# Kernel optimization log

Measured on AMD Instinct MI355X. Metric: run time of the kernel, lower is better.

The kernel has to match this reference:

```python
import jax, jax.numpy as jnp
import numpy as np

DIM = 1024
HEADS = 16
HIDDEN = 4096
EPS = 1e-5


def layernorm(x, w, b):
    mu = jnp.mean(x, axis=-1, keepdims=True)
    var = jnp.var(x, axis=-1, keepdims=True)
    return (x - mu) * jax.lax.rsqrt(var + EPS) * w + b


def setup_inputs() -> dict:
    key = jax.random.key(0)
    ks = jax.random.split(key, 12)
    s = lambda fan_in: 1.0 / np.sqrt(fan_in)
    return {
        "x": jax.random.normal(ks[0], (8, 1024, DIM), dtype=jnp.float32),
        "norm1_w": jnp.ones((DIM,), jnp.float32),
        "norm1_b": jnp.zeros((DIM,), jnp.float32),
        "qkv_w": jax.random.uniform(ks[1], (3 * DIM, DIM), jnp.float32, -s(DIM), s(DIM)),
        "proj_w": jax.random.uniform(ks[2], (DIM, DIM), jnp.float32, -s(DIM), s(DIM)),
        "proj_b": jax.random.uniform(ks[3], (DIM,), jnp.float32, -s(DIM), s(DIM)),
        "norm2_w": jnp.ones((DIM,), jnp.float32),
        "norm2_b": jnp.zeros((DIM,), jnp.float32),
        "fc1_w": jax.random.uniform(ks[4], (HIDDEN, DIM), jnp.float32, -s(DIM), s(DIM)),
        "fc1_b": jax.random.uniform(ks[5], (HIDDEN,), jnp.float32, -s(DIM), s(DIM)),
        "fc2_w": jax.random.uniform(ks[6], (DIM, HIDDEN), jnp.float32, -s(HIDDEN), s(HIDDEN)),
        "fc2_b": jax.random.uniform(ks[7], (DIM,), jnp.float32, -s(HIDDEN), s(HIDDEN)),
    }


def reference(x, norm1_w, norm1_b, qkv_w, proj_w, proj_b,
              norm2_w, norm2_b, fc1_w, fc1_b, fc2_w, fc2_b):
    B, N, C = x.shape
    hd = C // HEADS
    scale = hd ** -0.5

    # ---- attention branch ----
    xn = layernorm(x, norm1_w, norm1_b)
    qkv_tmp = jnp.einsum('bnc,oc->bno', xn, qkv_w)          # [B,N,3C]
    qkv = qkv_tmp.reshape(B, N, 3, HEADS, hd).transpose(2, 0, 3, 1, 4)
    q, k, v = qkv[0], qkv[1], qkv[2]                         # [B,H,N,hd]
    qkv_out = qkv_tmp.reshape(B, N, 3, C).transpose(2, 0, 1, 3)
    attn = jnp.einsum('bhnd,bhmd->bhnm', q, k) * scale       # [B,H,N,N]
    attn = jax.nn.softmax(attn, axis=-1)
    ao = jnp.einsum('bhnm,bhmd->bhnd', attn, v)              # [B,H,N,hd]
    ao = ao.transpose(0, 2, 1, 3).reshape(B, N, C)
    attn_out = jnp.einsum('bnc,oc->bno', ao, proj_w) + proj_b
    x = x + attn_out

    # ---- mlp branch ----
    xn2 = layernorm(x, norm2_w, norm2_b)
    h = jnp.einsum('bnc,hc->bnh', xn2, fc1_w) + fc1_b
    h = jax.nn.gelu(h, approximate=False)
    hidden_out = jnp.einsum('bnh,ch->bnc', h, fc2_w) + fc2_b
    x = x + hidden_out
    return (x, (qkv_out[0], qkv_out[1], qkv_out[2]), hidden_out)
```

## Files before the change

kernel.cpp:

```cpp
#include <hip/hip_runtime.h>
#include <hip/hip_bf16.h>

typedef __attribute__((ext_vector_type(8))) __bf16 bf16x8;
typedef __attribute__((ext_vector_type(4))) float f32x4;
typedef unsigned short u16;
typedef unsigned int u32;

#define TOK 8192
#define C_DIM 1024
#define OUT_SEC 8388608

__device__ __forceinline__ u16 f2bf(float f) {
  return __builtin_bit_cast(u16, __float2bfloat16(f));
}

__device__ __forceinline__ void gl_lds16(const void* g, void* l) {
  __builtin_amdgcn_global_load_lds(
      (__attribute__((address_space(1))) void*)const_cast<void*>(g),
      (__attribute__((address_space(3))) void*)l, 16, 0, 0);
}

__device__ __forceinline__ float gelu_f(float x) {
  float y = 0.7978845608f * (x + 0.044715f * x * x * x);
  y = fminf(fmaxf(y, -15.f), 15.f);
  float e = __expf(2.0f * y);
  float th = (e - 1.0f) / (e + 1.0f);
  return 0.5f * x * (1.0f + th);
}

__global__ __launch_bounds__(256) void cvt_kernel(const float* __restrict__ in,
                                                  u16* __restrict__ out, int n4) {
  int i = blockIdx.x * blockDim.x + threadIdx.x;
  if (i >= n4) return;
  float4 v = reinterpret_cast<const float4*>(in)[i];
  alignas(8) u16 pk[4];
  pk[0] = f2bf(v.x); pk[1] = f2bf(v.y); pk[2] = f2bf(v.z); pk[3] = f2bf(v.w);
  reinterpret_cast<uint2*>(out)[i] = *reinterpret_cast<uint2*>(pk);
}

__global__ __launch_bounds__(256) void ln_kernel(const float* __restrict__ x,
                                                 const float* __restrict__ w,
                                                 const float* __restrict__ b,
                                                 u16* __restrict__ out) {
  const int row = blockIdx.x;
  const int t = threadIdx.x;
  const float* xr = x + (size_t)row * C_DIM;
  float4 v = reinterpret_cast<const float4*>(xr)[t];
  float s = v.x + v.y + v.z + v.w;
  float ss = v.x * v.x + v.y * v.y + v.z * v.z + v.w * v.w;
#pragma unroll
  for (int off = 1; off < 64; off <<= 1) {
    s += __shfl_xor(s, off, 64);
    ss += __shfl_xor(ss, off, 64);
  }
  __shared__ float red[8];
  const int wv = t >> 6;
  if ((t & 63) == 0) { red[wv] = s; red[4 + wv] = ss; }
  __syncthreads();
  s = red[0] + red[1] + red[2] + red[3];
  ss = red[4] + red[5] + red[6] + red[7];
  const float mu = s * (1.0f / C_DIM);
  const float var = ss * (1.0f / C_DIM) - mu * mu;
  const float rstd = rsqrtf(var + 1e-5f);
  float4 w4 = reinterpret_cast<const float4*>(w)[t];
  float4 b4 = reinterpret_cast<const float4*>(b)[t];
  alignas(8) u16 pk[4];
  pk[0] = f2bf((v.x - mu) * rstd * w4.x + b4.x);
  pk[1] = f2bf((v.y - mu) * rstd * w4.y + b4.y);
  pk[2] = f2bf((v.z - mu) * rstd * w4.z + b4.z);
  pk[3] = f2bf((v.w - mu) * rstd * w4.w + b4.w);
  reinterpret_cast<uint2*>(out + (size_t)row * C_DIM)[t] = *reinterpret_cast<uint2*>(pk);
}

__global__ __launch_bounds__(256) void vtrans_kernel(const float* __restrict__ vsrc,
                                                     u16* __restrict__ vt) {
  const int bh = blockIdx.x, nt = blockIdx.y;
  const int b = bh >> 4, h = bh & 15;
  const int t = threadIdx.x;
  __shared__ u16 T[64][65];
#pragma unroll
  for (int p = 0; p < 4; ++p) {
    const int idx = p * 256 + t;
    const int n = idx >> 4, d4 = (idx & 15) * 4;
    float4 x4 = *reinterpret_cast<const float4*>(
        vsrc + (size_t)(b * 1024 + nt * 64 + n) * 1024 + h * 64 + d4);
    T[d4 + 0][n] = f2bf(x4.x);
    T[d4 + 1][n] = f2bf(x4.y);
    T[d4 + 2][n] = f2bf(x4.z);
    T[d4 + 3][n] = f2bf(x4.w);
  }
  __syncthreads();
  const int d = t >> 2, ns = (t & 3) * 16;
  u16* dst = vt + (size_t)bh * 65536 + (size_t)d * 1024 + nt * 64 + ns;
  alignas(16) u16 tmp[16];
#pragma unroll
  for (int i = 0; i < 16; ++i) tmp[i] = T[d][ns + i];
  reinterpret_cast<uint4*>(dst)[0] = reinterpret_cast<uint4*>(tmp)[0];
  reinterpret_cast<uint4*>(dst)[1] = reinterpret_cast<uint4*>(tmp)[1];
}

#define MFMA_T(AF, BF, BASE)                                                \
  _Pragma("unroll") for (int nf = 0; nf < 4; ++nf) {                        \
    _Pragma("unroll") for (int mf = 0; mf < 4; ++mf)                        \
        acc[(BASE) + mf][nf] = __builtin_amdgcn_mfma_f32_16x16x32_bf16(     \
            AF[mf], BF[nf], acc[(BASE) + mf][nf], 0, 0, 0);                 \
  }

enum { EPI8_QKV = 0, EPI8_FC1 = 1 };

template <int EPI>
__global__ __launch_bounds__(512, 2) void gemm8(
    const u16* __restrict__ A, const u16* __restrict__ Bw,
    const float* __restrict__ bias,
    float* __restrict__ out, u16* __restrict__ h1, u16* __restrict__ h2,
    int K) {
  extern __shared__ char smem[];
  const int t = threadIdx.x, lane = t & 63, wid = t >> 6;
  const int wm = wid >> 2, wn = wid & 3;

  const int nwg = gridDim.x;
  int lin = blockIdx.x;
  lin = (lin & 7) * (nwg >> 3) + (lin >> 3);
  const int brow0 = (lin & 31) * 256;
  const int bcol0 = (lin >> 5) * 256;

  const int NT = K >> 6;

  f32x4 zero = {0.f, 0.f, 0.f, 0.f};
  f32x4 acc[8][4];
#pragma unroll
  for (int m = 0; m < 8; ++m)
#pragma unroll
    for (int n = 0; n < 4; ++n) acc[m][n] = zero;

  const int src_slot = ((t & 3) ^ ((t >> 3) & 3)) * 8;
  const int srow = t >> 2;
  auto stage = [&](int buf, int mat, int ks, int ktile) {
    const u16* G = mat ? Bw : A;
    const int gr0 = mat ? bcol0 : brow0;
    const int k0 = ktile * 64 + ks * 32 + src_slot;
    char* dst = smem + ((buf << 16) | (mat << 15) | (ks << 14));
#pragma unroll
    for (int i = 0; i < 2; ++i)
      gl_lds16(G + (size_t)(gr0 + i * 128 + srow) * K + k0, dst + i * 8192 + t * 16);
  };

  const int swz16 = (((lane >> 4) ^ ((lane >> 1) & 3)) << 4);
  const int l15 = lane & 15;

  stage(0, 0, 0, 0);
  stage(0, 1, 0, 0);
  stage(0, 0, 1, 0);
  stage(0, 1, 1, 0);
  asm volatile("s_waitcnt vmcnt(4)" ::: "memory");
  __builtin_amdgcn_s_barrier();

  for (int tt = 0; tt < NT; ++tt) {
    char* As_ = smem + ((tt & 1) << 16);
    char* Bs_ = As_ + 32768;
    const int nbuf = (tt & 1) ^ 1;
    const bool pf = (tt + 1 < NT);
    bf16x8 af[4], af2[4], bfr[4];

    auto LDA = [&](bf16x8* dst8, int MH, int KK) {
#pragma unroll
      for (int mf = 0; mf < 4; ++mf)
        dst8[mf] = *reinterpret_cast<const bf16x8*>(
            As_ + KK * 16384 + (wm * 128 + MH * 64 + mf * 16 + l15) * 64 + swz16);
    };
    auto LDB = [&](int KK) {
#pragma unroll
      for (int nf = 0; nf < 4; ++nf)
        bfr[nf] = *reinterpret_cast<const bf16x8*>(
            Bs_ + KK * 16384 + (wn * 64 + nf * 16 + l15) * 64 + swz16);
    };

    LDB(0);
    LDA(af, 0, 0);
    __builtin_amdgcn_sched_barrier(0);
    LDA(af2, 1, 0);
    __builtin_amdgcn_sched_barrier(0);
    if (pf) { stage(nbuf, 0, 0, tt + 1); stage(nbuf, 1, 0, tt + 1); }
    asm volatile("s_waitcnt lgkmcnt(4)" ::: "memory");
    __builtin_amdgcn_sched_barrier(0);
    __builtin_amdgcn_s_setprio(1);
    MFMA_T(af, bfr, 0)
    asm volatile("s_waitcnt lgkmcnt(0)" ::: "memory");
    __builtin_amdgcn_sched_barrier(0);
    MFMA_T(af2, bfr, 4)
    __builtin_amdgcn_s_setprio(0);
    if (pf) {
      asm volatile("s_waitcnt vmcnt(4)" ::: "memory");
    } else {
      asm volatile("s_waitcnt vmcnt(0)" ::: "memory");
    }
    __builtin_amdgcn_s_barrier();

    LDB(1);
    LDA(af, 1, 1);
    __builtin_amdgcn_sched_barrier(0);
    LDA(af2, 0, 1);
    __builtin_amdgcn_sched_barrier(0);
    if (pf) { stage(nbuf, 0, 1, tt + 1); stage(nbuf, 1, 1, tt + 1); }
    asm volatile("s_waitcnt lgkmcnt(4)" ::: "memory");
    __builtin_amdgcn_sched_barrier(0);
    __builtin_amdgcn_s_setprio(1);
    MFMA_T(af, bfr, 4)
    asm volatile("s_waitcnt lgkmcnt(0)" ::: "memory");
    __builtin_amdgcn_sched_barrier(0);
    MFMA_T(af2, bfr, 0)
    __builtin_amdgcn_s_setprio(0);
    if (pf)
      asm volatile("s_waitcnt vmcnt(4)" ::: "memory");
    __builtin_amdgcn_s_barrier();
  }

  const int rb = brow0 + wm * 128;
  const int cb = bcol0 + wn * 64;
#pragma unroll
  for (int m = 0; m < 8; ++m) {
#pragma unroll
    for (int n = 0; n < 4; ++n) {
      const int c = cb + n * 16 + l15;
#pragma unroll
      for (int j = 0; j < 4; ++j) {
        const int r = rb + m * 16 + (lane >> 4) * 4 + j;
        float v = acc[m][n][j];
        if constexpr (EPI == EPI8_QKV) {
          const int sec = c >> 10, cc = c & 1023;
          out[(size_t)sec * OUT_SEC + (size_t)r * 1024 + cc] = v;
          const size_t boff =
              (((size_t)(r >> 10) * 16 + (cc >> 6)) * 1024 + (r & 1023)) * 64 + (cc & 63);
          if (sec == 0) h1[boff] = f2bf(v * 0.18033688f);
          else if (sec == 1) h2[boff] = f2bf(v);
        } else {
          v += bias[c];
          h1[(size_t)r * 4096 + c] = f2bf(gelu_f(v));
        }
      }
    }
  }
}

enum { EPIN_PROJ = 0, EPIN_FC2 = 1 };

template <int EPI>
__global__ __launch_bounds__(512, 1) void gemm8n(
    const u16* __restrict__ A, const u16* __restrict__ Bw,
    const float* __restrict__ bias, const float* resid,
    float* out, float* out2_f, int K) {
  extern __shared__ char smem[];
  const int t = threadIdx.x, lane = t & 63, wid = t >> 6;
  const int wm = wid >> 2, wn = wid & 3;

  const int nwg = gridDim.x;
  int lin = blockIdx.x;
  lin = (lin & 7) * (nwg >> 3) + (lin >> 3);
  const int brow0 = (lin & 63) * 128;
  const int bcol0 = (lin >> 6) * 256;

  const int NT = K >> 6;

  f32x4 zero = {0.f, 0.f, 0.f, 0.f};
  f32x4 acc[4][4];
#pragma unroll
  for (int m = 0; m < 4; ++m)
#pragma unroll
    for (int n = 0; n < 4; ++n) acc[m][n] = zero;

  const int src_slot = ((t & 3) ^ ((t >> 3) & 3)) * 8;
  const int srow = t >> 2;
  auto stage_all = [&](char* dst, int ktile) {
#pragma unroll
    for (int ks = 0; ks < 2; ++ks) {
      const int k0 = ktile * 64 + ks * 32 + src_slot;
      gl_lds16(A + (size_t)(brow0 + srow) * K + k0, dst + ks * 8192 + t * 16);
    }
#pragma unroll
    for (int ks = 0; ks < 2; ++ks) {
      const int k0 = ktile * 64 + ks * 32 + src_slot;
      char* db = dst + 16384 + ks * 16384;
#pragma unroll
      for (int i = 0; i < 2; ++i)
        gl_lds16(Bw + (size_t)(bcol0 + i * 128 + srow) * K + k0, db + i * 8192 + t * 16);
    }
  };

  const int swz16 = (((lane >> 4) ^ ((lane >> 1) & 3)) << 4);
  const int l15 = lane & 15;

  char* bcur = smem;
  char* bnxt = smem + 49152;
  char* bspr = smem + 98304;

  stage_all(bcur, 0);
  stage_all(bnxt, 1);
  asm volatile("s_waitcnt vmcnt(6)" ::: "memory");
  __builtin_amdgcn_s_barrier();

  for (int tt = 0; tt < NT; ++tt) {
    const bool pf2 = (tt + 2 < NT);
    bf16x8 af[4], af2[4], bfr[4], bfr2[4];

    auto LDA = [&](bf16x8* dst8, int KK) {
#pragma unroll
      for (int mf = 0; mf < 4; ++mf)
        dst8[mf] = *reinterpret_cast<const bf16x8*>(
            bcur + KK * 8192 + (wm * 64 + mf * 16 + l15) * 64 + swz16);
    };
    auto LDB = [&](bf16x8* dst8, int KK) {
#pragma unroll
      for (int nf = 0; nf < 4; ++nf)
        dst8[nf] = *reinterpret_cast<const bf16x8*>(
            bcur + 16384 + KK * 16384 + (wn * 64 + nf * 16 + l15) * 64 + swz16);
    };

    LDA(af, 0);
    LDB(bfr, 0);
    __builtin_amdgcn_sched_barrier(0);
    LDA(af2, 1);
    LDB(bfr2, 1);
    __builtin_amdgcn_sched_barrier(0);
    if (pf2) stage_all(bspr, tt + 2);
    asm volatile("s_waitcnt lgkmcnt(8)" ::: "memory");
    __builtin_amdgcn_sched_barrier(0);
    __builtin_amdgcn_s_setprio(1);
    MFMA_T(af, bfr, 0)
    asm volatile("s_waitcnt lgkmcnt(0)" ::: "memory");
    __builtin_amdgcn_sched_barrier(0);
    MFMA_T(af2, bfr2, 0)
    __builtin_amdgcn_s_setprio(0);
    if (pf2) {
      asm volatile("s_waitcnt vmcnt(6)" ::: "memory");
    } else {
      asm volatile("s_waitcnt vmcnt(0)" ::: "memory");
    }
    __builtin_amdgcn_s_barrier();

    char* tmp = bcur;
    bcur = bnxt;
    bnxt = bspr;
    bspr = tmp;
  }

  const int rb = brow0 + wm * 64;
  const int cb = bcol0 + wn * 64;
#pragma unroll
  for (int m = 0; m < 4; ++m) {
#pragma unroll
    for (int n = 0; n < 4; ++n) {
      const int c = cb + n * 16 + l15;
#pragma unroll
      for (int j = 0; j < 4; ++j) {
        const int r = rb + m * 16 + (lane >> 4) * 4 + j;
        float v = acc[m][n][j];
        if constexpr (EPI == EPIN_PROJ) {
          v += bias[c] + resid[(size_t)r * 1024 + c];
          out[(size_t)r * 1024 + c] = v;
        } else {
          v += bias[c];
          out[(size_t)r * 1024 + c] = v;
          out2_f[(size_t)r * 1024 + c] = resid[(size_t)r * 1024 + c] + v;
        }
      }
    }
  }
}

__global__ __launch_bounds__(256) void attn_kernel(const u16* __restrict__ Qb,
                                                   const u16* __restrict__ Kb,
                                                   const u16* __restrict__ Vtb,
                                                   u16* __restrict__ ao) {
  const int orig = blockIdx.y * gridDim.x + blockIdx.x;
  const int wid = (orig & 7) * 256 + (orig >> 3);
  const int bh = wid >> 4;
  const int qt = wid & 15;
  const int b = bh >> 4, h = bh & 15;
  const int t = threadIdx.x, lane = t & 63, wv = t >> 6;
  const int l15 = lane & 15, g = lane >> 4;

  __shared__ u16 Ks[2][4096];
  __shared__ u16 Vs[2][4096];

  const int q0 = qt * 64 + wv * 16;
  bf16x8 qf[2];
#pragma unroll
  for (int c = 0; c < 2; ++c)
    qf[c] = *reinterpret_cast<const bf16x8*>(
        Qb + (size_t)bh * 65536 + (size_t)(q0 + l15) * 64 + c * 32 + g * 8);

  f32x4 zero = {0.f, 0.f, 0.f, 0.f};
  f32x4 accO[4];
#pragma unroll
  for (int nb = 0; nb < 4; ++nb) accO[nb] = zero;
  float m = -1e30f, lrun = 0.f;

  const char* ktile0 = (const char*)(Kb + (size_t)bh * 65536);
  const char* vbase = (const char*)(Vtb + (size_t)bh * 65536);

  auto stage = [&](int buf, int kv0) {
#pragma unroll
    for (int i = 0; i < 2; ++i) {
      const int o = i * 4096 + t * 16;
      const int row = o >> 7, colb = o & 127;
      const int swz = colb ^ ((row & 7) << 4);
      gl_lds16(ktile0 + (size_t)kv0 * 128 + (size_t)row * 128 + swz, (char*)Ks[buf] + o);
      gl_lds16(vbase + (size_t)row * 2048 + (size_t)kv0 * 2 + swz, (char*)Vs[buf] + o);
    }
  };

  stage(0, 0);
  __syncthreads();
  int cur = 0;

  const int a0 = (l15 + ((g & 1) << 5)) << 2;
  const int a1 = a0 + 64;
  const bool up = (lane & 32) != 0;

  for (int tile = 0; tile < 16; ++tile) {
    if (tile < 15) stage(cur ^ 1, (tile + 1) * 64);

    f32x4 sacc[4];
#pragma unroll
    for (int jb = 0; jb < 4; ++jb) sacc[jb] = zero;
#pragma unroll
    for (int jb = 0; jb < 4; ++jb)
#pragma unroll
      for (int c = 0; c < 2; ++c) {
        const int row = jb * 16 + l15;
        const int colb = c * 64 + g * 16;
        bf16x8 kf = *reinterpret_cast<const bf16x8*>(
            (const char*)Ks[cur] + row * 128 + (colb ^ ((row & 7) << 4)));
        sacc[jb] = __builtin_amdgcn_mfma_f32_16x16x32_bf16(kf, qf[c], sacc[jb], 0, 0, 0);
      }

    float mt = sacc[0][0];
#pragma unroll
    for (int jb = 0; jb < 4; ++jb)
#pragma unroll
      for (int r = 0; r < 4; ++r) mt = fmaxf(mt, sacc[jb][r]);
    mt = fmaxf(mt, __shfl_xor(mt, 16, 64));
    mt = fmaxf(mt, __shfl_xor(mt, 32, 64));

    if (!__all(mt <= m + 8.0f)) {
      const float mn = fmaxf(m, mt);
      const float sc = exp2f(m - mn);
      lrun *= sc;
#pragma unroll
      for (int nb = 0; nb < 4; ++nb) accO[nb] *= sc;
      m = mn;
    }

    float rs = 0.f;
#pragma unroll
    for (int jb = 0; jb < 4; ++jb)
#pragma unroll
      for (int r = 0; r < 4; ++r) {
        const float p = exp2f(sacc[jb][r] - m);
        sacc[jb][r] = p;
        rs += p;
      }
    rs += __shfl_xor(rs, 16, 64);
    rs += __shfl_xor(rs, 32, 64);
    lrun += rs;

    int w[4][2];
#pragma unroll
    for (int jb = 0; jb < 4; ++jb) {
      w[jb][0] = (int)((u32)f2bf(sacc[jb][0]) | ((u32)f2bf(sacc[jb][1]) << 16));
      w[jb][1] = (int)((u32)f2bf(sacc[jb][2]) | ((u32)f2bf(sacc[jb][3]) << 16));
    }

#pragma unroll
    for (int c = 0; c < 2; ++c) {
      int lo0 = __builtin_amdgcn_ds_bpermute(a0, w[2 * c][0]);
      int hi0 = __builtin_amdgcn_ds_bpermute(a0, w[2 * c + 1][0]);
      int lo1 = __builtin_amdgcn_ds_bpermute(a0, w[2 * c][1]);
      int hi1 = __builtin_amdgcn_ds_bpermute(a0, w[2 * c + 1][1]);
      int lo2 = __builtin_amdgcn_ds_bpermute(a1, w[2 * c][0]);
      int hi2 = __builtin_amdgcn_ds_bpermute(a1, w[2 * c + 1][0]);
      int lo3 = __builtin_amdgcn_ds_bpermute(a1, w[2 * c][1]);
      int hi3 = __builtin_amdgcn_ds_bpermute(a1, w[2 * c + 1][1]);
      alignas(16) int word[4] = {up ? hi0 : lo0, up ? hi1 : lo1,
                                 up ? hi2 : lo2, up ? hi3 : lo3};
      bf16x8 pfB = *reinterpret_cast<bf16x8*>(word);
#pragma unroll
      for (int nb = 0; nb < 4; ++nb) {
        const int row = nb * 16 + l15;
        const int colb = c * 64 + g * 16;
        bf16x8 vf = *reinterpret_cast<const bf16x8*>(
            (const char*)Vs[cur] + row * 128 + (colb ^ ((row & 7) << 4)));
        accO[nb] = __builtin_amdgcn_mfma_f32_16x16x32_bf16(vf, pfB, accO[nb], 0, 0, 0);
      }
    }

    __syncthreads();
    cur ^= 1;
  }

  const float rl = __builtin_amdgcn_rcpf(lrun);
  u16* dst = ao + (size_t)(b * 1024 + q0 + l15) * 1024 + h * 64 + g * 4;
#pragma unroll
  for (int nb = 0; nb < 4; ++nb) {
    alignas(8) u16 pk[4];
#pragma unroll
    for (int j = 0; j < 4; ++j) pk[j] = f2bf(accO[nb][j] * rl);
    *reinterpret_cast<uint2*>(dst + nb * 16) = *reinterpret_cast<uint2*>(pk);
  }
}

extern "C" void kernel_launch(void* const* d_in, const int* in_sizes, int n_in,
                              void* d_out, int out_size, void* d_ws, size_t ws_size,
                              hipStream_t stream) {
  const float* x      = (const float*)d_in[0];
  const float* n1w    = (const float*)d_in[1];
  const float* n1b    = (const float*)d_in[2];
  const float* qkv_w  = (const float*)d_in[3];
  const float* proj_w = (const float*)d_in[4];
  const float* proj_b = (const float*)d_in[5];
  const float* n2w    = (const float*)d_in[6];
  const float* n2b    = (const float*)d_in[7];
  const float* fc1_w  = (const float*)d_in[8];
  const float* fc1_b  = (const float*)d_in[9];
  const float* fc2_w  = (const float*)d_in[10];
  const float* fc2_b  = (const float*)d_in[11];
  float* out = (float*)d_out;

  u16* wsb    = (u16*)d_ws;
  u16* w_qkv  = wsb;
  u16* w_proj = wsb + 3145728;
  u16* w_fc1  = wsb + 4194304;
  u16* w_fc2  = wsb + 8388608;
  u16* xn     = wsb + 12582912;
  u16* Qb     = wsb + 20971520;
  u16* Kb     = wsb + 29360128;
  u16* Vtw    = wsb + 37748736;
  u16* ao     = wsb + 46137344;
  u16* hbuf   = wsb + 20971520;

  (void)hipFuncSetAttribute((const void*)gemm8<EPI8_QKV>,
                            hipFuncAttributeMaxDynamicSharedMemorySize, 131072);
  (void)hipFuncSetAttribute((const void*)gemm8<EPI8_FC1>,
                            hipFuncAttributeMaxDynamicSharedMemorySize, 131072);
  (void)hipFuncSetAttribute((const void*)gemm8n<EPIN_PROJ>,
                            hipFuncAttributeMaxDynamicSharedMemorySize, 147456);
  (void)hipFuncSetAttribute((const void*)gemm8n<EPIN_FC2>,
                            hipFuncAttributeMaxDynamicSharedMemorySize, 147456);

  cvt_kernel<<<3072, 256, 0, stream>>>(qkv_w, w_qkv, 786432);
  cvt_kernel<<<1024, 256, 0, stream>>>(proj_w, w_proj, 262144);
  cvt_kernel<<<4096, 256, 0, stream>>>(fc1_w, w_fc1, 1048576);
  cvt_kernel<<<4096, 256, 0, stream>>>(fc2_w, w_fc2, 1048576);

  ln_kernel<<<TOK, 256, 0, stream>>>(x, n1w, n1b, xn);
  gemm8<EPI8_QKV><<<384, 512, 131072, stream>>>(
      xn, w_qkv, nullptr, out + OUT_SEC, Qb, Kb, 1024);
  vtrans_kernel<<<dim3(128, 16), 256, 0, stream>>>(out + 3 * (size_t)OUT_SEC, Vtw);
  attn_kernel<<<dim3(128, 16), 256, 0, stream>>>(Qb, Kb, Vtw, ao);
  gemm8n<EPIN_PROJ><<<256, 512, 147456, stream>>>(
      ao, w_proj, proj_b, x, out, nullptr, 1024);
  ln_kernel<<<TOK, 256, 0, stream>>>(out, n2w, n2b, xn);
  gemm8<EPI8_FC1><<<512, 512, 131072, stream>>>(
      xn, w_fc1, fc1_b, nullptr, hbuf, nullptr, 1024);
  gemm8n<EPIN_FC2><<<256, 512, 147456, stream>>>(
      hbuf, w_fc2, fc2_b, out, out + 4 * (size_t)OUT_SEC, out, 4096);
}
```

Measured before the change: 440.1 us.

## Process two query blocks per wave and triple-buffer KV tiles in attention

Each wave now handles 32 query rows instead of 16, so every K and V fragment read from LDS feeds two MFMAs. Block count halves to match. KV staging goes from double to triple buffering with explicit vmcnt waits and raw barriers, so loads run two tiles ahead. The row-sum shuffles move out of the loop and run once at the end. This costs more registers and LDS per block, which may lower occupancy.

```diff
diff --git a/kernel.cpp b/kernel.cpp
--- a/kernel.cpp
+++ b/kernel.cpp
@@ -372,45 +372,51 @@
                                                    const u16* __restrict__ Vtb,
                                                    u16* __restrict__ ao) {
   const int orig = blockIdx.y * gridDim.x + blockIdx.x;
-  const int wid = (orig & 7) * 256 + (orig >> 3);
-  const int bh = wid >> 4;
-  const int qt = wid & 15;
+  const int wid = (orig & 7) * 128 + (orig >> 3);
+  const int bh = wid >> 3;
+  const int qt = wid & 7;
   const int b = bh >> 4, h = bh & 15;
   const int t = threadIdx.x, lane = t & 63, wv = t >> 6;
   const int l15 = lane & 15, g = lane >> 4;
 
-  __shared__ u16 Ks[2][4096];
-  __shared__ u16 Vs[2][4096];
-
-  const int q0 = qt * 64 + wv * 16;
-  bf16x8 qf[2];
-#pragma unroll
-  for (int c = 0; c < 2; ++c)
-    qf[c] = *reinterpret_cast<const bf16x8*>(
+  __shared__ u16 KV[3][8192];
+
+  const int q0 = qt * 128 + wv * 32;
+  bf16x8 qfA[2], qfB[2];
+#pragma unroll
+  for (int c = 0; c < 2; ++c) {
+    qfA[c] = *reinterpret_cast<const bf16x8*>(
         Qb + (size_t)bh * 65536 + (size_t)(q0 + l15) * 64 + c * 32 + g * 8);
+    qfB[c] = *reinterpret_cast<const bf16x8*>(
+        Qb + (size_t)bh * 65536 + (size_t)(q0 + 16 + l15) * 64 + c * 32 + g * 8);
+  }
+  asm volatile("s_waitcnt vmcnt(0)" ::: "memory");
 
   f32x4 zero = {0.f, 0.f, 0.f, 0.f};
-  f32x4 accO[4];
-#pragma unroll
-  for (int nb = 0; nb < 4; ++nb) accO[nb] = zero;
-  float m = -1e30f, lrun = 0.f;
+  f32x4 accO0[4], accO1[4];
+#pragma unroll
+  for (int nb = 0; nb < 4; ++nb) { accO0[nb] = zero; accO1[nb] = zero; }
+  float m0 = -1e30f, m1 = -1e30f, lr0 = 0.f, lr1 = 0.f;
 
   const char* ktile0 = (const char*)(Kb + (size_t)bh * 65536);
   const char* vbase = (const char*)(Vtb + (size_t)bh * 65536);
 
   auto stage = [&](int buf, int kv0) {
+    char* base = (char*)KV[buf];
 #pragma unroll
     for (int i = 0; i < 2; ++i) {
       const int o = i * 4096 + t * 16;
       const int row = o >> 7, colb = o & 127;
       const int swz = colb ^ ((row & 7) << 4);
-      gl_lds16(ktile0 + (size_t)kv0 * 128 + (size_t)row * 128 + swz, (char*)Ks[buf] + o);
-      gl_lds16(vbase + (size_t)row * 2048 + (size_t)kv0 * 2 + swz, (char*)Vs[buf] + o);
+      gl_lds16(ktile0 + (size_t)kv0 * 128 + (size_t)row * 128 + swz, base + o);
+      gl_lds16(vbase + (size_t)row * 2048 + (size_t)kv0 * 2 + swz, base + 8192 + o);
     }
   };
 
   stage(0, 0);
-  __syncthreads();
+  stage(1, 64);
+  asm volatile("s_waitcnt vmcnt(4)" ::: "memory");
+  __builtin_amdgcn_s_barrier();
   int cur = 0;
 
   const int a0 = (l15 + ((g & 1) << 5)) << 2;
@@ -418,11 +424,19 @@
   const bool up = (lane & 32) != 0;
 
   for (int tile = 0; tile < 16; ++tile) {
-    if (tile < 15) stage(cur ^ 1, (tile + 1) * 64);
-
-    f32x4 sacc[4];
-#pragma unroll
-    for (int jb = 0; jb < 4; ++jb) sacc[jb] = zero;
+    const bool pf2 = (tile + 2 < 16);
+    if (pf2) {
+      int spare = cur + 2;
+      if (spare >= 3) spare -= 3;
+      stage(spare, (tile + 2) * 64);
+    }
+
+    const char* kcur = (const char*)KV[cur];
+    const char* vcur = kcur + 8192;
+
+    f32x4 s0[4], s1[4];
+#pragma unroll
+    for (int jb = 0; jb < 4; ++jb) { s0[jb] = zero; s1[jb] = zero; }
 #pragma unroll
     for (int jb = 0; jb < 4; ++jb)
 #pragma unroll
@@ -430,82 +444,142 @@
         const int row = jb * 16 + l15;
         const int colb = c * 64 + g * 16;
         bf16x8 kf = *reinterpret_cast<const bf16x8*>(
-            (const char*)Ks[cur] + row * 128 + (colb ^ ((row & 7) << 4)));
-        sacc[jb] = __builtin_amdgcn_mfma_f32_16x16x32_bf16(kf, qf[c], sacc[jb], 0, 0, 0);
-      }
-
-    float mt = sacc[0][0];
-#pragma unroll
-    for (int jb = 0; jb < 4; ++jb)
-#pragma unroll
-      for (int r = 0; r < 4; ++r) mt = fmaxf(mt, sacc[jb][r]);
-    mt = fmaxf(mt, __shfl_xor(mt, 16, 64));
-    mt = fmaxf(mt, __shfl_xor(mt, 32, 64));
-
-    if (!__all(mt <= m + 8.0f)) {
-      const float mn = fmaxf(m, mt);
-      const float sc = exp2f(m - mn);
-      lrun *= sc;
-#pragma unroll
-      for (int nb = 0; nb < 4; ++nb) accO[nb] *= sc;
-      m = mn;
-    }
-
-    float rs = 0.f;
-#pragma unroll
-    for (int jb = 0; jb < 4; ++jb)
-#pragma unroll
-      for (int r = 0; r < 4; ++r) {
-        const float p = exp2f(sacc[jb][r] - m);
-        sacc[jb][r] = p;
-        rs += p;
-      }
-    rs += __shfl_xor(rs, 16, 64);
-    rs += __shfl_xor(rs, 32, 64);
-    lrun += rs;
-
-    int w[4][2];
-#pragma unroll
-    for (int jb = 0; jb < 4; ++jb) {
-      w[jb][0] = (int)((u32)f2bf(sacc[jb][0]) | ((u32)f2bf(sacc[jb][1]) << 16));
-      w[jb][1] = (int)((u32)f2bf(sacc[jb][2]) | ((u32)f2bf(sacc[jb][3]) << 16));
+            kcur + row * 128 + (colb ^ ((row & 7) << 4)));
+        s0[jb] = __builtin_amdgcn_mfma_f32_16x16x32_bf16(kf, qfA[c], s0[jb], 0, 0, 0);
+        s1[jb] = __builtin_amdgcn_mfma_f32_16x16x32_bf16(kf, qfB[c], s1[jb], 0, 0, 0);
+      }
+
+    int w0[4][2], w1[4][2];
+    {
+      float a = fmaxf(fmaxf(s0[0][0], s0[0][1]), fmaxf(s0[0][2], s0[0][3]));
+      float bmx = fmaxf(fmaxf(s0[1][0], s0[1][1]), fmaxf(s0[1][2], s0[1][3]));
+      float cmx = fmaxf(fmaxf(s0[2][0], s0[2][1]), fmaxf(s0[2][2], s0[2][3]));
+      float dmx = fmaxf(fmaxf(s0[3][0], s0[3][1]), fmaxf(s0[3][2], s0[3][3]));
+      float mt = fmaxf(fmaxf(a, bmx), fmaxf(cmx, dmx));
+      mt = fmaxf(mt, __shfl_xor(mt, 16, 64));
+      mt = fmaxf(mt, __shfl_xor(mt, 32, 64));
+      if (!__all(mt <= m0 + 8.0f)) {
+        const float mn = fmaxf(m0, mt);
+        const float sc = exp2f(m0 - mn);
+        lr0 *= sc;
+#pragma unroll
+        for (int nb = 0; nb < 4; ++nb) accO0[nb] *= sc;
+        m0 = mn;
+      }
+      float rs = 0.f;
+#pragma unroll
+      for (int jb = 0; jb < 4; ++jb)
+#pragma unroll
+        for (int r = 0; r < 4; ++r) {
+          const float p = exp2f(s0[jb][r] - m0);
+          s0[jb][r] = p;
+          rs += p;
+        }
+      lr0 += rs;
+#pragma unroll
+      for (int jb = 0; jb < 4; ++jb) {
+        w0[jb][0] = (int)((u32)f2bf(s0[jb][0]) | ((u32)f2bf(s0[jb][1]) << 16));
+        w0[jb][1] = (int)((u32)f2bf(s0[jb][2]) | ((u32)f2bf(s0[jb][3]) << 16));
+      }
+    }
+    {
+      float a = fmaxf(fmaxf(s1[0][0], s1[0][1]), fmaxf(s1[0][2], s1[0][3]));
+      float bmx = fmaxf(fmaxf(s1[1][0], s1[1][1]), fmaxf(s1[1][2], s1[1][3]));
+      float cmx = fmaxf(fmaxf(s1[2][0], s1[2][1]), fmaxf(s1[2][2], s1[2][3]));
+      float dmx = fmaxf(fmaxf(s1[3][0], s1[3][1]), fmaxf(s1[3][2], s1[3][3]));
+      float mt = fmaxf(fmaxf(a, bmx), fmaxf(cmx, dmx));
+      mt = fmaxf(mt, __shfl_xor(mt, 16, 64));
+      mt = fmaxf(mt, __shfl_xor(mt, 32, 64));
+      if (!__all(mt <= m1 + 8.0f)) {
+        const float mn = fmaxf(m1, mt);
+        const float sc = exp2f(m1 - mn);
+        lr1 *= sc;
+#pragma unroll
+        for (int nb = 0; nb < 4; ++nb) accO1[nb] *= sc;
+        m1 = mn;
+      }
+      float rs = 0.f;
+#pragma unroll
+      for (int jb = 0; jb < 4; ++jb)
+#pragma unroll
+        for (int r = 0; r < 4; ++r) {
+          const float p = exp2f(s1[jb][r] - m1);
+          s1[jb][r] = p;
+          rs += p;
+        }
+      lr1 += rs;
+#pragma unroll
+      for (int jb = 0; jb < 4; ++jb) {
+        w1[jb][0] = (int)((u32)f2bf(s1[jb][0]) | ((u32)f2bf(s1[jb][1]) << 16));
+        w1[jb][1] = (int)((u32)f2bf(s1[jb][2]) | ((u32)f2bf(s1[jb][3]) << 16));
+      }
     }
 
 #pragma unroll
     for (int c = 0; c < 2; ++c) {
-      int lo0 = __builtin_amdgcn_ds_bpermute(a0, w[2 * c][0]);
-      int hi0 = __builtin_amdgcn_ds_bpermute(a0, w[2 * c + 1][0]);
-      int lo1 = __builtin_amdgcn_ds_bpermute(a0, w[2 * c][1]);
-      int hi1 = __builtin_amdgcn_ds_bpermute(a0, w[2 * c + 1][1]);
-      int lo2 = __builtin_amdgcn_ds_bpermute(a1, w[2 * c][0]);
-      int hi2 = __builtin_amdgcn_ds_bpermute(a1, w[2 * c + 1][0]);
-      int lo3 = __builtin_amdgcn_ds_bpermute(a1, w[2 * c][1]);
-      int hi3 = __builtin_amdgcn_ds_bpermute(a1, w[2 * c + 1][1]);
-      alignas(16) int word[4] = {up ? hi0 : lo0, up ? hi1 : lo1,
-                                 up ? hi2 : lo2, up ? hi3 : lo3};
-      bf16x8 pfB = *reinterpret_cast<bf16x8*>(word);
+      int p0w0 = __builtin_amdgcn_ds_bpermute(a0, w0[2 * c][0]);
+      int p0w0h = __builtin_amdgcn_ds_bpermute(a0, w0[2 * c + 1][0]);
+      int p0w1 = __builtin_amdgcn_ds_bpermute(a0, w0[2 * c][1]);
+      int p0w1h = __builtin_amdgcn_ds_bpermute(a0, w0[2 * c + 1][1]);
+      int p0w2 = __builtin_amdgcn_ds_bpermute(a1, w0[2 * c][0]);
+      int p0w2h = __builtin_amdgcn_ds_bpermute(a1, w0[2 * c + 1][0]);
+      int p0w3 = __builtin_amdgcn_ds_bpermute(a1, w0[2 * c][1]);
+      int p0w3h = __builtin_amdgcn_ds_bpermute(a1, w0[2 * c + 1][1]);
+      alignas(16) int word0[4] = {up ? p0w0h : p0w0, up ? p0w1h : p0w1,
+                                  up ? p0w2h : p0w2, up ? p0w3h : p0w3};
+      bf16x8 pf0 = *reinterpret_cast<bf16x8*>(word0);
+
+      int p1w0 = __builtin_amdgcn_ds_bpermute(a0, w1[2 * c][0]);
+      int p1w0h = __builtin_amdgcn_ds_bpermute(a0, w1[2 * c + 1][0]);
+      int p1w1 = __builtin_amdgcn_ds_bpermute(a0, w1[2 * c][1]);
+      int p1w1h = __builtin_amdgcn_ds_bpermute(a0, w1[2 * c + 1][1]);
+      int p1w2 = __builtin_amdgcn_ds_bpermute(a1, w1[2 * c][0]);
+      int p1w2h = __builtin_amdgcn_ds_bpermute(a1, w1[2 * c + 1][0]);
+      int p1w3 = __builtin_amdgcn_ds_bpermute(a1, w1[2 * c][1]);
+      int p1w3h = __builtin_amdgcn_ds_bpermute(a1, w1[2 * c + 1][1]);
+      alignas(16) int word1[4] = {up ? p1w0h : p1w0, up ? p1w1h : p1w1,
+                                  up ? p1w2h : p1w2, up ? p1w3h : p1w3};
+      bf16x8 pf1 = *reinterpret_cast<bf16x8*>(word1);
+
 #pragma unroll
       for (int nb = 0; nb < 4; ++nb) {
         const int row = nb * 16 + l15;
         const int colb = c * 64 + g * 16;
         bf16x8 vf = *reinterpret_cast<const bf16x8*>(
-            (const char*)Vs[cur] + row * 128 + (colb ^ ((row & 7) << 4)));
-        accO[nb] = __builtin_amdgcn_mfma_f32_16x16x32_bf16(vf, pfB, accO[nb], 0, 0, 0);
-      }
-    }
-
-    __syncthreads();
-    cur ^= 1;
-  }
-
-  const float rl = __builtin_amdgcn_rcpf(lrun);
-  u16* dst = ao + (size_t)(b * 1024 + q0 + l15) * 1024 + h * 64 + g * 4;
+            vcur + row * 128 + (colb ^ ((row & 7) << 4)));
+        accO0[nb] = __builtin_amdgcn_mfma_f32_16x16x32_bf16(vf, pf0, accO0[nb], 0, 0, 0);
+        accO1[nb] = __builtin_amdgcn_mfma_f32_16x16x32_bf16(vf, pf1, accO1[nb], 0, 0, 0);
+      }
+    }
+
+    if (pf2) {
+      asm volatile("s_waitcnt vmcnt(4)" ::: "memory");
+    } else {
+      asm volatile("s_waitcnt vmcnt(0)" ::: "memory");
+    }
+    __builtin_amdgcn_s_barrier();
+    cur = (cur == 2) ? 0 : cur + 1;
+  }
+
+  lr0 += __shfl_xor(lr0, 16, 64);
+  lr0 += __shfl_xor(lr0, 32, 64);
+  lr1 += __shfl_xor(lr1, 16, 64);
+  lr1 += __shfl_xor(lr1, 32, 64);
+  const float rl0 = __builtin_amdgcn_rcpf(lr0);
+  const float rl1 = __builtin_amdgcn_rcpf(lr1);
+
+  u16* dst0 = ao + (size_t)(b * 1024 + q0 + l15) * 1024 + h * 64 + g * 4;
+  u16* dst1 = ao + (size_t)(b * 1024 + q0 + 16 + l15) * 1024 + h * 64 + g * 4;
 #pragma unroll
   for (int nb = 0; nb < 4; ++nb) {
-    alignas(8) u16 pk[4];
-#pragma unroll
-    for (int j = 0; j < 4; ++j) pk[j] = f2bf(accO[nb][j] * rl);
-    *reinterpret_cast<uint2*>(dst + nb * 16) = *reinterpret_cast<uint2*>(pk);
+    alignas(8) u16 pk0[4], pk1[4];
+#pragma unroll
+    for (int j = 0; j < 4; ++j) {
+      pk0[j] = f2bf(accO0[nb][j] * rl0);
+      pk1[j] = f2bf(accO1[nb][j] * rl1);
+    }
+    *reinterpret_cast<uint2*>(dst0 + nb * 16) = *reinterpret_cast<uint2*>(pk0);
+    *reinterpret_cast<uint2*>(dst1 + nb * 16) = *reinterpret_cast<uint2*>(pk1);
   }
 }
 
@@ -556,7 +630,7 @@
   gemm8<EPI8_QKV><<<384, 512, 131072, stream>>>(
       xn, w_qkv, nullptr, out + OUT_SEC, Qb, Kb, 1024);
   vtrans_kernel<<<dim3(128, 16), 256, 0, stream>>>(out + 3 * (size_t)OUT_SEC, Vtw);
-  attn_kernel<<<dim3(128, 16), 256, 0, stream>>>(Qb, Kb, Vtw, ao);
+  attn_kernel<<<dim3(128, 8), 256, 0, stream>>>(Qb, Kb, Vtw, ao);
   gemm8n<EPIN_PROJ><<<256, 512, 147456, stream>>>(
       ao, w_proj, proj_b, x, out, nullptr, 1024);
   ln_kernel<<<TOK, 256, 0, stream>>>(out, n2w, n2b, xn);
```

New measurement: 441.5 us. No clear change (+0.3%).
